# Kernel tuning notes

Measured on AMD Instinct MI355X. Metric: run time of the kernel, lower is better.

## Reference

```python
import jax, jax.numpy as jnp
import numpy as np

EPS = 1e-4

def setup_inputs() -> dict:
    key = jax.random.key(0)
    x = jax.random.normal(key, (32, 512, 4000), dtype=jnp.float32)
    return {"x": x}

def reference(x):
    # x: [batch, bins, frames]; causal cumulative normalization along frames
    frames = x.shape[-1]
    count = jnp.arange(1, frames + 1, dtype=x.dtype).reshape(1, 1, frames)
    cum_sum = jnp.cumsum(x, axis=-1)
    cum_pow_sum = jnp.cumsum(x * x, axis=-1)
    cum_mean = cum_sum / count
    cum_var = cum_pow_sum / count - cum_mean * cum_mean
    cum_std = jnp.sqrt(cum_var + EPS)
    return (x - cum_mean) / cum_std
```

## Files before the change

kernel.cpp:

```cpp
#include <hip/hip_runtime.h>

#define EPS 1e-4f
#define FRAMES 4000
#define TPB 256
#define VPT 4
#define EPT (VPT * 4)
#define ACTIVE_T (FRAMES / EPT)

__global__ __launch_bounds__(TPB) void cumnorm_kernel(const float* __restrict__ x,
                                                      float* __restrict__ out,
                                                      int rows) {
    const int row  = blockIdx.x;
    if (row >= rows) return;
    const int t    = threadIdx.x;
    const int wave = t >> 6;
    const int lane = t & 63;

    const float4* __restrict__ xr = (const float4*)(x + (size_t)row * FRAMES);
    float4* __restrict__ outr     = (float4*)(out + (size_t)row * FRAMES);

    const bool active = (t < ACTIVE_T);

    float4 v[VPT];
    if (active) {
        #pragma unroll
        for (int j = 0; j < VPT; ++j) v[j] = xr[t * VPT + j];
    } else {
        #pragma unroll
        for (int j = 0; j < VPT; ++j) v[j] = make_float4(0.f, 0.f, 0.f, 0.f);
    }

    float S = 0.f, Q = 0.f;
    #pragma unroll
    for (int j = 0; j < VPT; ++j) {
        S += v[j].x; Q = fmaf(v[j].x, v[j].x, Q);
        S += v[j].y; Q = fmaf(v[j].y, v[j].y, Q);
        S += v[j].z; Q = fmaf(v[j].z, v[j].z, Q);
        S += v[j].w; Q = fmaf(v[j].w, v[j].w, Q);
    }

    float ss = S, qq = Q;
    #pragma unroll
    for (int d = 1; d < 64; d <<= 1) {
        const float us = __shfl_up(ss, d, 64);
        const float uq = __shfl_up(qq, d, 64);
        if (lane >= d) { ss += us; qq += uq; }
    }

    __shared__ float wsum[4];
    __shared__ float wsq[4];
    if (lane == 63) { wsum[wave] = ss; wsq[wave] = qq; }
    __syncthreads();

    float cs = ss - S;
    float cq = qq - Q;
    #pragma unroll
    for (int w = 0; w < 3; ++w) {
        if (w < wave) { cs += wsum[w]; cq += wsq[w]; }
    }

    if (active) {
        const float nbase = (float)(t * EPT);
        #pragma unroll
        for (int j = 0; j < VPT; ++j) {
            float4 r;
            {
                cs += v[j].x; cq = fmaf(v[j].x, v[j].x, cq);
                const float inv  = __builtin_amdgcn_rcpf(nbase + (float)(j * 4 + 1));
                const float mean = cs * inv;
                const float var  = fmaf(-mean, mean, cq * inv);
                r.x = (v[j].x - mean) * __builtin_amdgcn_rsqf(var + EPS);
            }
            {
                cs += v[j].y; cq = fmaf(v[j].y, v[j].y, cq);
                const float inv  = __builtin_amdgcn_rcpf(nbase + (float)(j * 4 + 2));
                const float mean = cs * inv;
                const float var  = fmaf(-mean, mean, cq * inv);
                r.y = (v[j].y - mean) * __builtin_amdgcn_rsqf(var + EPS);
            }
            {
                cs += v[j].z; cq = fmaf(v[j].z, v[j].z, cq);
                const float inv  = __builtin_amdgcn_rcpf(nbase + (float)(j * 4 + 3));
                const float mean = cs * inv;
                const float var  = fmaf(-mean, mean, cq * inv);
                r.z = (v[j].z - mean) * __builtin_amdgcn_rsqf(var + EPS);
            }
            {
                cs += v[j].w; cq = fmaf(v[j].w, v[j].w, cq);
                const float inv  = __builtin_amdgcn_rcpf(nbase + (float)(j * 4 + 4));
                const float mean = cs * inv;
                const float var  = fmaf(-mean, mean, cq * inv);
                r.w = (v[j].w - mean) * __builtin_amdgcn_rsqf(var + EPS);
            }
            outr[t * VPT + j] = r;
        }
    }
}

extern "C" void kernel_launch(void* const* d_in, const int* in_sizes, int n_in,
                              void* d_out, int out_size, void* d_ws, size_t ws_size,
                              hipStream_t stream) {
    const float* x = (const float*)d_in[0];
    float* out = (float*)d_out;
    const int rows = in_sizes[0] / FRAMES;

    dim3 grid(rows);
    dim3 block(TPB);
    cumnorm_kernel<<<grid, block, 0, stream>>>(x, out, rows);
}
```

Baseline: 433.3 us.

## Interleave float4 chunks across threads for coalesced loads with four parallel scans

Each thread now owns one float4 in each of four block-strided chunks instead of four consecutive float4s, so every global load and store instruction covers a contiguous run across the wave. The per-thread prefix scan becomes four independent scans whose wave and block totals are chained through shared memory to build exclusive carries. This targets memory transaction efficiency on a bandwidth-bound kernel. The cost is four times the shuffle and shared-memory scan work.

Measured after the change: 423.8 us. 1.02x faster.

```diff
diff --git a/kernel.cpp b/kernel.cpp
--- a/kernel.cpp
+++ b/kernel.cpp
@@ -3,9 +3,9 @@
 #define EPS 1e-4f
 #define FRAMES 4000
 #define TPB 256
-#define VPT 4
-#define EPT (VPT * 4)
-#define ACTIVE_T (FRAMES / EPT)
+#define NV (FRAMES / 4)
+#define NCHUNK 4
+#define LAST_ACT (NV - 3 * TPB)
 
 __global__ __launch_bounds__(TPB) void cumnorm_kernel(const float* __restrict__ x,
                                                       float* __restrict__ out,
@@ -19,81 +19,102 @@
     const float4* __restrict__ xr = (const float4*)(x + (size_t)row * FRAMES);
     float4* __restrict__ outr     = (float4*)(out + (size_t)row * FRAMES);
 
-    const bool active = (t < ACTIVE_T);
+    const bool act3 = (t < LAST_ACT);
 
-    float4 v[VPT];
-    if (active) {
-        #pragma unroll
-        for (int j = 0; j < VPT; ++j) v[j] = xr[t * VPT + j];
-    } else {
-        #pragma unroll
-        for (int j = 0; j < VPT; ++j) v[j] = make_float4(0.f, 0.f, 0.f, 0.f);
+    float4 v[NCHUNK];
+    v[0] = xr[t];
+    v[1] = xr[TPB + t];
+    v[2] = xr[2 * TPB + t];
+    v[3] = act3 ? xr[3 * TPB + t] : make_float4(0.f, 0.f, 0.f, 0.f);
+
+    float S[NCHUNK], Q[NCHUNK];
+    #pragma unroll
+    for (int k = 0; k < NCHUNK; ++k) {
+        float s = v[k].x;            float q = v[k].x * v[k].x;
+        s += v[k].y;                 q = fmaf(v[k].y, v[k].y, q);
+        s += v[k].z;                 q = fmaf(v[k].z, v[k].z, q);
+        s += v[k].w;                 q = fmaf(v[k].w, v[k].w, q);
+        S[k] = s; Q[k] = q;
     }
 
-    float S = 0.f, Q = 0.f;
+    float ss[NCHUNK], qq[NCHUNK];
     #pragma unroll
-    for (int j = 0; j < VPT; ++j) {
-        S += v[j].x; Q = fmaf(v[j].x, v[j].x, Q);
-        S += v[j].y; Q = fmaf(v[j].y, v[j].y, Q);
-        S += v[j].z; Q = fmaf(v[j].z, v[j].z, Q);
-        S += v[j].w; Q = fmaf(v[j].w, v[j].w, Q);
+    for (int k = 0; k < NCHUNK; ++k) { ss[k] = S[k]; qq[k] = Q[k]; }
+    #pragma unroll
+    for (int d = 1; d < 64; d <<= 1) {
+        float us[NCHUNK], uq[NCHUNK];
+        #pragma unroll
+        for (int k = 0; k < NCHUNK; ++k) {
+            us[k] = __shfl_up(ss[k], d, 64);
+            uq[k] = __shfl_up(qq[k], d, 64);
+        }
+        if (lane >= d) {
+            #pragma unroll
+            for (int k = 0; k < NCHUNK; ++k) { ss[k] += us[k]; qq[k] += uq[k]; }
+        }
     }
 
-    float ss = S, qq = Q;
-    #pragma unroll
-    for (int d = 1; d < 64; d <<= 1) {
-        const float us = __shfl_up(ss, d, 64);
-        const float uq = __shfl_up(qq, d, 64);
-        if (lane >= d) { ss += us; qq += uq; }
+    __shared__ float wt_s[NCHUNK][4];
+    __shared__ float wt_q[NCHUNK][4];
+    if (lane == 63) {
+        #pragma unroll
+        for (int k = 0; k < NCHUNK; ++k) { wt_s[k][wave] = ss[k]; wt_q[k][wave] = qq[k]; }
+    }
+    __syncthreads();
+
+    float excl_s[NCHUNK], excl_q[NCHUNK];
+    {
+        float carry_s = 0.f, carry_q = 0.f;
+        #pragma unroll
+        for (int k = 0; k < NCHUNK; ++k) {
+            float wp_s = 0.f, wp_q = 0.f, ct_s = 0.f, ct_q = 0.f;
+            #pragma unroll
+            for (int w = 0; w < 4; ++w) {
+                const float a = wt_s[k][w], b = wt_q[k][w];
+                ct_s += a; ct_q += b;
+                if (w < wave) { wp_s += a; wp_q += b; }
+            }
+            excl_s[k] = carry_s + wp_s + (ss[k] - S[k]);
+            excl_q[k] = carry_q + wp_q + (qq[k] - Q[k]);
+            carry_s += ct_s; carry_q += ct_q;
+        }
     }
 
-    __shared__ float wsum[4];
-    __shared__ float wsq[4];
-    if (lane == 63) { wsum[wave] = ss; wsq[wave] = qq; }
-    __syncthreads();
-
-    float cs = ss - S;
-    float cq = qq - Q;
     #pragma unroll
-    for (int w = 0; w < 3; ++w) {
-        if (w < wave) { cs += wsum[w]; cq += wsq[w]; }
-    }
-
-    if (active) {
-        const float nbase = (float)(t * EPT);
-        #pragma unroll
-        for (int j = 0; j < VPT; ++j) {
-            float4 r;
-            {
-                cs += v[j].x; cq = fmaf(v[j].x, v[j].x, cq);
-                const float inv  = __builtin_amdgcn_rcpf(nbase + (float)(j * 4 + 1));
-                const float mean = cs * inv;
-                const float var  = fmaf(-mean, mean, cq * inv);
-                r.x = (v[j].x - mean) * __builtin_amdgcn_rsqf(var + EPS);
-            }
-            {
-                cs += v[j].y; cq = fmaf(v[j].y, v[j].y, cq);
-                const float inv  = __builtin_amdgcn_rcpf(nbase + (float)(j * 4 + 2));
-                const float mean = cs * inv;
-                const float var  = fmaf(-mean, mean, cq * inv);
-                r.y = (v[j].y - mean) * __builtin_amdgcn_rsqf(var + EPS);
-            }
-            {
-                cs += v[j].z; cq = fmaf(v[j].z, v[j].z, cq);
-                const float inv  = __builtin_amdgcn_rcpf(nbase + (float)(j * 4 + 3));
-                const float mean = cs * inv;
-                const float var  = fmaf(-mean, mean, cq * inv);
-                r.z = (v[j].z - mean) * __builtin_amdgcn_rsqf(var + EPS);
-            }
-            {
-                cs += v[j].w; cq = fmaf(v[j].w, v[j].w, cq);
-                const float inv  = __builtin_amdgcn_rcpf(nbase + (float)(j * 4 + 4));
-                const float mean = cs * inv;
-                const float var  = fmaf(-mean, mean, cq * inv);
-                r.w = (v[j].w - mean) * __builtin_amdgcn_rsqf(var + EPS);
-            }
-            outr[t * VPT + j] = r;
+    for (int k = 0; k < NCHUNK; ++k) {
+        if (k == 3 && !act3) break;
+        float cs = excl_s[k], cq = excl_q[k];
+        const float nbase = (float)((k * TPB + t) << 2);
+        float4 r;
+        {
+            cs += v[k].x; cq = fmaf(v[k].x, v[k].x, cq);
+            const float inv  = __builtin_amdgcn_rcpf(nbase + 1.0f);
+            const float mean = cs * inv;
+            const float var  = fmaf(-mean, mean, cq * inv);
+            r.x = (v[k].x - mean) * __builtin_amdgcn_rsqf(var + EPS);
         }
+        {
+            cs += v[k].y; cq = fmaf(v[k].y, v[k].y, cq);
+            const float inv  = __builtin_amdgcn_rcpf(nbase + 2.0f);
+            const float mean = cs * inv;
+            const float var  = fmaf(-mean, mean, cq * inv);
+            r.y = (v[k].y - mean) * __builtin_amdgcn_rsqf(var + EPS);
+        }
+        {
+            cs += v[k].z; cq = fmaf(v[k].z, v[k].z, cq);
+            const float inv  = __builtin_amdgcn_rcpf(nbase + 3.0f);
+            const float mean = cs * inv;
+            const float var  = fmaf(-mean, mean, cq * inv);
+            r.z = (v[k].z - mean) * __builtin_amdgcn_rsqf(var + EPS);
+        }
+        {
+            cs += v[k].w; cq = fmaf(v[k].w, v[k].w, cq);
+            const float inv  = __builtin_amdgcn_rcpf(nbase + 4.0f);
+            const float mean = cs * inv;
+            const float var  = fmaf(-mean, mean, cq * inv);
+            r.w = (v[k].w - mean) * __builtin_amdgcn_rsqf(var + EPS);
+        }
+        outr[k * TPB + t] = r;
     }
 }
 
@@ -104,7 +125,5 @@
     float* out = (float*)d_out;
     const int rows = in_sizes[0] / FRAMES;
 
-    dim3 grid(rows);
-    dim3 block(TPB);
-    cumnorm_kernel<<<grid, block, 0, stream>>>(x, out, rows);
+    cumnorm_kernel<<<dim3(rows), dim3(TPB), 0, stream>>>(x, out, rows);
 }
```
